# Kernel optimization log

Measured on AMD Instinct MI355X. Metric: run time of the kernel, lower is better.

Reference implementation:

```python
import jax, jax.numpy as jnp
import numpy as np

N, E = 20000, 4096
IN_DIM, DET_DIM, HID, OUT = 512, 256, 256, 2
HALF = HID // 2
EPS = 1e-6


def setup_inputs() -> dict:
    key = jax.random.key(0)
    ks = jax.random.split(key, 20)
    g = lambda k, shape, fan_in: jax.random.normal(k, shape, jnp.float32) / np.sqrt(fan_in)
    return {
        "x": jax.random.normal(ks[0], (N, IN_DIM), jnp.float32),
        "z": jax.random.normal(ks[1], (N, DET_DIM), jnp.float32),
        "incidence": jax.random.uniform(ks[2], (N, E), jnp.float32),
        "edge_weights": jax.random.uniform(ks[3], (E,), jnp.float32),
        "psi_w": g(ks[4], (IN_DIM, HALF), IN_DIM), "psi_b": jnp.zeros((HALF,), jnp.float32),
        "phi_w": g(ks[5], (DET_DIM, HALF), DET_DIM), "phi_b": jnp.zeros((HALF,), jnp.float32),
        "g1_w": g(ks[6], (2 * HALF, HID), 2 * HALF), "g1_b": jnp.zeros((HID,), jnp.float32),
        "g2_w": g(ks[7], (HID, HALF), HID), "g2_b": jnp.zeros((HALF,), jnp.float32),
        "th1": g(ks[8], (HALF, HID), HALF), "b1": jnp.zeros((HID,), jnp.float32),
        "th2": g(ks[9], (HID, HID), HID), "b2": jnp.zeros((HID,), jnp.float32),
        "out_w": g(ks[10], (HID, OUT), HID), "out_b": jnp.zeros((OUT,), jnp.float32),
    }


def hconv(X, H, w, theta, bias):
    # HGNN-style message passing: Dv^{-1/2} H W De^{-1} H^T Dv^{-1/2} (X theta) + b
    Xt = X @ theta                              # [N,F]
    De = H.sum(axis=0)                          # [E] edge degree
    Dv = H @ w                                  # [N] weighted node degree
    inv_sqrt_dv = jax.lax.rsqrt(jnp.maximum(Dv, EPS))[:, None]
    He = H.T @ (Xt * inv_sqrt_dv)               # [E,F] gather to hyperedges
    He = He * (w / jnp.maximum(De, EPS))[:, None]
    return (H @ He) * inv_sqrt_dv + bias        # scatter back to nodes


def reference(x, z, incidence, edge_weights,
              psi_w, psi_b, phi_w, phi_b,
              g1_w, g1_b, g2_w, g2_b,
              th1, b1, th2, b2, out_w, out_b):
    proj_x = x @ psi_w + psi_b                  # [N,HALF]
    proj_z = z @ phi_w + phi_b                  # [N,HALF]
    cat = jnp.concatenate([proj_x, proj_z], axis=1)
    gate = jax.nn.sigmoid(jax.nn.relu(cat @ g1_w + g1_b) @ g2_w + g2_b)
    fused = gate * proj_z + (1.0 - gate) * proj_x
    h = jax.nn.relu(hconv(fused, incidence, edge_weights, th1, b1))
    h = jax.nn.relu(hconv(h, incidence, edge_weights, th2, b2))
    logits = h @ out_w + out_b                  # [N,OUT]
    return logits, gate
```

## Files before the change

kernel.cpp:

```cpp
#include <hip/hip_runtime.h>
#include <hip/hip_bf16.h>


typedef __bf16 bf16_t;
typedef __attribute__((ext_vector_type(8))) __bf16 bf16x8;
typedef __attribute__((ext_vector_type(4))) __bf16 bf16x4;
typedef __attribute__((ext_vector_type(4))) float f32x4;

#define NN 20000
#define NE 4096
#define NNP 20480
#define AT_S 16
#define NEB 16
#define NNB 160

__device__ __forceinline__ f32x4 mfma16(bf16x8 a, bf16x8 b, f32x4 c) {
  return __builtin_amdgcn_mfma_f32_16x16x32_bf16(a, b, c, 0, 0, 0);
}

__global__ __launch_bounds__(256) void stats_cvt_kern(const float* __restrict__ H,
                                                      const float* __restrict__ w,
                                                      float* __restrict__ Dvp,
                                                      float* __restrict__ Dep,
                                                      bf16_t* __restrict__ Hbp) {
  __shared__ float dvl2[128][65];
  __shared__ float deP[4][256];
  int t = threadIdx.x, l = t & 63, wv = t >> 6;
  long e0 = (long)blockIdx.x * 256;
  long n0 = (long)blockIdx.y * 128;
  long pbase = ((e0 >> 6) + (l >> 4)) * (long)NNP;
  int inner = (l & 15) * 4;
  f32x4 w4 = *(const f32x4*)(w + e0 + l * 4);
  f32x4 de; de[0] = de[1] = de[2] = de[3] = 0.f;
  #pragma unroll 4
  for (int i = 0; i < 32; ++i) {
    long row = n0 + wv * 32 + i;
    float s;
    if (row < NN) {
      f32x4 u = *(const f32x4*)(H + row * NE + e0 + l * 4);
      bf16x4 pk;
      #pragma unroll
      for (int j = 0; j < 4; ++j) pk[j] = (__bf16)u[j];
      *(bf16x4*)(Hbp + (pbase + row) * 64 + inner) = pk;
      de += u;
      s = u[0] * w4[0] + u[1] * w4[1] + u[2] * w4[2] + u[3] * w4[3];
    } else {
      bf16x4 z;
      #pragma unroll
      for (int j = 0; j < 4; ++j) z[j] = (__bf16)0.f;
      *(bf16x4*)(Hbp + (pbase + row) * 64 + inner) = z;
      s = 0.f;
    }
    dvl2[wv * 32 + i][l] = s;
  }
  *(f32x4*)(&deP[wv][l * 4]) = de;
  __syncthreads();
  {
    int row = t >> 1, hf = t & 1;
    float s = 0.f;
    #pragma unroll
    for (int j = 0; j < 32; ++j) s += dvl2[row][hf * 32 + j];
    s += __shfl_xor(s, 1);
    if (hf == 0) Dvp[(long)blockIdx.x * NNP + n0 + row] = s;
  }
  {
    float s = deP[0][t] + deP[1][t] + deP[2][t] + deP[3][t];
    Dep[(long)blockIdx.y * NE + e0 + t] = s;
  }
}

__global__ __launch_bounds__(256) void finalize_kern(const float* __restrict__ Dvp,
                                                     const float* __restrict__ Dep,
                                                     const float* __restrict__ w,
                                                     float* __restrict__ isd,
                                                     float* __restrict__ es) {
  int t = blockIdx.x * 256 + threadIdx.x;
  if (t < NN) {
    float s = 0.f;
    #pragma unroll 8
    for (int b = 0; b < NEB; ++b) s += Dvp[(long)b * NNP + t];
    isd[t] = rsqrtf(fmaxf(s, 1e-6f));
  }
  if (t < NE) {
    float s = 0.f;
    #pragma unroll 8
    for (int b = 0; b < NNB; ++b) s += Dep[(long)b * NE + t];
    es[t] = w[t] / fmaxf(s, 1e-6f);
  }
}

__global__ void cvtw_kern(const float* __restrict__ psi, const float* __restrict__ phi,
                          const float* __restrict__ g1,  const float* __restrict__ g2,
                          const float* __restrict__ th1, const float* __restrict__ th2,
                          bf16_t* dpsi, bf16_t* dphi, bf16_t* dg1, bf16_t* dg2,
                          bf16_t* dth1, bf16_t* dth2) {
  int t = blockIdx.x * 256 + threadIdx.x;
  if (t < 65536) {
    int nc = t >> 9, k = t & 511; dpsi[t] = (__bf16)psi[k * 128 + nc];
  } else if (t < 98304) {
    int i = t - 65536; int nc = i >> 8, k = i & 255; dphi[i] = (__bf16)phi[k * 128 + nc];
  } else if (t < 163840) {
    int i = t - 98304; int nc = i >> 8, k = i & 255; dg1[i] = (__bf16)g1[k * 256 + nc];
  } else if (t < 196608) {
    int i = t - 163840; int nc = i >> 8, k = i & 255; dg2[i] = (__bf16)g2[k * 128 + nc];
  } else if (t < 229376) {
    int i = t - 196608; int nc = i >> 7, k = i & 127; dth1[i] = (__bf16)th1[k * 256 + nc];
  } else if (t < 294912) {
    int i = t - 229376; int nc = i >> 8, k = i & 255; dth2[i] = (__bf16)th2[k * 256 + nc];
  }
}

enum { EPI_CAT = 0, EPI_RELU = 1 };

template<bool AF32, int EPI>
__global__ __launch_bounds__(256) void gemm_node_kern(
    const void* __restrict__ Av, int lda, const bf16_t* __restrict__ Bt, int K,
    const float* __restrict__ bias, bf16_t* __restrict__ dst, int ldc) {
  int tid = threadIdx.x, l = tid & 63, wv = tid >> 6;
  int lr = l & 15, lq = l >> 4;
  int hm = wv >> 1;
  int mo = blockIdx.x * 32 + hm * 16;
  int no = blockIdx.y * 128 + (wv & 1) * 64;
  f32x4 acc[4] = {};
  for (int k0 = 0; k0 < K; k0 += 32) {
    int row = mo + lr;
    bf16x8 a;
    if (row < NN) {
      if constexpr (AF32) {
        const float* ap = (const float*)Av + (long)row * lda + k0 + lq * 8;
        f32x4 u0 = *(const f32x4*)ap, u1 = *(const f32x4*)(ap + 4);
        #pragma unroll
        for (int j = 0; j < 4; ++j) { a[j] = (__bf16)u0[j]; a[j + 4] = (__bf16)u1[j]; }
      } else {
        a = *(const bf16x8*)((const bf16_t*)Av + (long)row * lda + k0 + lq * 8);
      }
    } else {
      #pragma unroll
      for (int j = 0; j < 8; ++j) a[j] = (__bf16)0.f;
    }
    #pragma unroll
    for (int ni = 0; ni < 4; ++ni) {
      bf16x8 b = *(const bf16x8*)(Bt + (long)(no + ni * 16 + lr) * K + k0 + lq * 8);
      acc[ni] = mfma16(a, b, acc[ni]);
    }
  }
  #pragma unroll
  for (int ni = 0; ni < 4; ++ni) {
    int colf = no + ni * 16 + lr;
    int rb = mo + lq * 4;
    f32x4 v = acc[ni];
    float bs = bias[colf];
    for (int r = 0; r < 4; ++r) {
      int n = rb + r;
      if (n < NN) {
        float xx = v[r] + bs;
        if constexpr (EPI == EPI_RELU) xx = xx > 0.f ? xx : 0.f;
        dst[(long)n * ldc + colf] = (__bf16)xx;
      }
    }
  }
}

__global__ __launch_bounds__(256) void gate_y_kern(
    const bf16_t* __restrict__ hid1, const bf16_t* __restrict__ g2w,
    const float* __restrict__ g2b, const bf16_t* __restrict__ cat,
    const bf16_t* __restrict__ th1w, const float* __restrict__ isd,
    float* __restrict__ gate_out, bf16_t* __restrict__ Yf) {
  __shared__ bf16_t fl[32 * 132];
  int t = threadIdx.x, l = t & 63, wv = t >> 6;
  int lr = l & 15, lq = l >> 4;
  if (blockIdx.x >= 625) {
    bf16x8 z;
    #pragma unroll
    for (int j = 0; j < 8; ++j) z[j] = (__bf16)0.f;
    #pragma unroll
    for (int i = 0; i < 4; ++i)
      *(bf16x8*)(Yf + (((long)(wv + i * 4) * 640 + blockIdx.x) * 64 + l) * 8) = z;
    return;
  }
  long n0 = (long)blockIdx.x * 32;
  int hm = wv >> 1, nq = wv & 1;
  int mo = hm * 16, no = nq * 64;
  f32x4 acc[4] = {};
  for (int k0 = 0; k0 < 256; k0 += 32) {
    bf16x8 a = *(const bf16x8*)(hid1 + (n0 + mo + lr) * 256 + k0 + lq * 8);
    #pragma unroll
    for (int ni = 0; ni < 4; ++ni) {
      bf16x8 b = *(const bf16x8*)(g2w + (long)(no + ni * 16 + lr) * 256 + k0 + lq * 8);
      acc[ni] = mfma16(a, b, acc[ni]);
    }
  }
  #pragma unroll
  for (int ni = 0; ni < 4; ++ni) {
    int colf = no + ni * 16 + lr;
    float bs = g2b[colf];
    #pragma unroll
    for (int r = 0; r < 4; ++r) {
      long n = n0 + mo + lq * 4 + r;
      float g = 1.f / (1.f + __expf(-(acc[ni][r] + bs)));
      gate_out[n * 128 + colf] = g;
      float px = (float)cat[n * 256 + colf];
      float pz = (float)cat[n * 256 + 128 + colf];
      fl[(mo + lq * 4 + r) * 132 + colf] = (__bf16)(g * pz + (1.f - g) * px);
    }
  }
  __syncthreads();
  int hm2 = wv >> 1, f128 = (wv & 1) * 128;
  f32x4 acc2[8] = {};
  for (int k0 = 0; k0 < 128; k0 += 32) {
    bf16x8 a = *(const bf16x8*)(fl + (hm2 * 16 + lr) * 132 + k0 + lq * 8);
    #pragma unroll
    for (int ni = 0; ni < 8; ++ni) {
      bf16x8 b = *(const bf16x8*)(th1w + (long)(f128 + ni * 16 + lr) * 128 + k0 + lq * 8);
      acc2[ni] = mfma16(a, b, acc2[ni]);
    }
  }
  int lanep = (hm2 * 2 + (lq >> 1)) * 16 + lr;
  #pragma unroll
  for (int ni = 0; ni < 8; ++ni) {
    int fblk = (f128 >> 4) + ni;
    bf16x4 pk;
    #pragma unroll
    for (int r = 0; r < 4; ++r) {
      long n = n0 + hm2 * 16 + lq * 4 + r;
      pk[r] = (__bf16)(acc2[ni][r] * isd[n]);
    }
    *(bf16x4*)(Yf + (((long)fblk * 640 + blockIdx.x) * 64 + lanep) * 8 + (lq & 1) * 4) = pk;
  }
}

__global__ __launch_bounds__(512) void at_gemm_kern(const bf16_t* __restrict__ Hbp,
                                                    const bf16_t* __restrict__ Yf,
                                                    bf16_t* __restrict__ part) {
  __shared__ bf16_t T[128 * 72];
  int t = threadIdx.x, l = t & 63, wv = t >> 6;
  int lr = l & 15, lq = l >> 4;
  int eh = wv >> 2, fq = wv & 3;
  int e0 = blockIdx.x * 128;
  int s0 = blockIdx.y * 20, s1 = s0 + 20;
  int rp = t >> 4;
  int ck = t & 15;
  f32x4 acc[4][4] = {};
  const bf16_t* src = Hbp + (((long)(e0 >> 6) + (ck >> 3)) * NNP + (long)s0 * 64 + 2 * rp) * 64
                          + (ck & 7) * 8;
  bf16x8 ra = *(const bf16x8*)src;
  bf16x8 rb = *(const bf16x8*)(src + 64);
  for (int s = s0; s < s1; ++s) {
    __syncthreads();
    #pragma unroll
    for (int j = 0; j < 8; ++j) {
      int jj = (j + ck) & 7;
      int el = ck * 8 + jj;
      unsigned lo = (unsigned)__builtin_bit_cast(unsigned short, (__bf16)ra[jj]);
      unsigned hi = (unsigned)__builtin_bit_cast(unsigned short, (__bf16)rb[jj]);
      *(unsigned*)(T + el * 72 + rp * 2) = lo | (hi << 16);
    }
    __syncthreads();
    if (s + 1 < s1) {
      src += 64 * 64;
      ra = *(const bf16x8*)src;
      rb = *(const bf16x8*)(src + 64);
    }
    #pragma unroll
    for (int k32 = 0; k32 < 2; ++k32) {
      bf16x8 a[4], b[4];
      #pragma unroll
      for (int ni = 0; ni < 4; ++ni)
        a[ni] = *(const bf16x8*)(T + (eh * 64 + ni * 16 + lr) * 72 + k32 * 32 + lq * 8);
      const bf16_t* bp = Yf + ((long)(s * 2 + k32) * 64 + l) * 8;
      #pragma unroll
      for (int ni = 0; ni < 4; ++ni)
        b[ni] = *(const bf16x8*)(bp + (long)(fq * 4 + ni) * 640 * 512);
      #pragma unroll
      for (int ae = 0; ae < 4; ++ae)
        #pragma unroll
        for (int bf = 0; bf < 4; ++bf)
          acc[ae][bf] = mfma16(a[ae], b[bf], acc[ae][bf]);
    }
  }
  bf16_t* pp = part + (long)blockIdx.y * (256 * 4096);
  #pragma unroll
  for (int ae = 0; ae < 4; ++ae) {
    int eblk16 = (e0 >> 4) + eh * 4 + ae;
    #pragma unroll
    for (int bf = 0; bf < 4; ++bf) {
      int fblk = fq * 4 + bf;
      f32x4 v = acc[ae][bf];
      bf16x4 pk;
      for (int r = 0; r < 4; ++r) pk[r] = (__bf16)v[r];
      *(bf16x4*)(pp + (((long)eblk16 * 16 + fblk) * 64 + l) * 4) = pk;
    }
  }
}

__global__ __launch_bounds__(256) void reduce_he(const bf16_t* __restrict__ part,
                                                 const float* __restrict__ es,
                                                 bf16_t* __restrict__ Hef) {
  int u = blockIdx.x * 256 + threadIdx.x;
  int lane = u & 63, tile = u >> 6;
  int fblk = tile & 15, eblk16 = tile >> 4;
  int lr = lane & 15, lq = lane >> 4;
  int e_base = eblk16 * 16 + lq * 4;
  float a0 = 0.f, a1 = 0.f, a2 = 0.f, a3 = 0.f;
  #pragma unroll
  for (int s = 0; s < AT_S; ++s) {
    bf16x4 v = *(const bf16x4*)(part + (long)s * (256 * 4096) + (long)u * 4);
    a0 += (float)v[0]; a1 += (float)v[1]; a2 += (float)v[2]; a3 += (float)v[3];
  }
  f32x4 e4 = *(const f32x4*)(es + e_base);
  bf16x4 pk;
  pk[0] = (__bf16)(a0 * e4[0]); pk[1] = (__bf16)(a1 * e4[1]);
  pk[2] = (__bf16)(a2 * e4[2]); pk[3] = (__bf16)(a3 * e4[3]);
  int eblk32 = eblk16 >> 1;
  int lanep = ((eblk16 & 1) * 2 + (lq >> 1)) * 16 + lr;
  long slot = (((long)fblk * 128 + eblk32) * 64 + lanep) * 8 + (lq & 1) * 4;
  *(bf16x4*)(Hef + slot) = pk;
}

template<int CONV>
__global__ __launch_bounds__(512) void out_gemm_kern(const bf16_t* __restrict__ Hef,
                                                     const bf16_t* __restrict__ Hbp,
                                                     const float* __restrict__ isd,
                                                     const float* __restrict__ bias,
                                                     const bf16_t* __restrict__ th2w,
                                                     bf16_t* __restrict__ Yf,
                                                     const float* __restrict__ ow,
                                                     const float* __restrict__ ob,
                                                     float* __restrict__ out) {
  __shared__ bf16_t lbuf[2][4096];
  __shared__ float lgp[8][64][2];
  __shared__ bf16_t hl[64 * 260];
  int t = threadIdx.x, l = t & 63, wv = t >> 6;
  int lr = l & 15, lq = l >> 4;
  long r0 = (long)blockIdx.x * 64;
  f32x4 acc[4][2] = {};
  const bf16_t* asrc = Hbp + (r0 + (wv >> 1) * 16 + lr) * 64 + (wv & 1) * 32 + lq * 8;
  const bf16_t* bbase = Hef + (long)l * 8;
  bf16x8 rg = *(const bf16x8*)asrc;
  int c = 0;
  for (int s = 0; s < 64; ++s) {
    *(bf16x8*)(&lbuf[c][wv * 512 + l * 8]) = rg;
    __syncthreads();
    if (s + 1 < 64) rg = *(const bf16x8*)(asrc + (long)(s + 1) * NNP * 64);
    #pragma unroll
    for (int k32 = 0; k32 < 2; ++k32) {
      bf16x8 a[4], b[2];
      #pragma unroll
      for (int mi = 0; mi < 4; ++mi)
        a[mi] = *(const bf16x8*)(&lbuf[c][(mi * 2 + k32) * 512 + l * 8]);
      int eblk = s * 2 + k32;
      #pragma unroll
      for (int ni = 0; ni < 2; ++ni)
        b[ni] = *(const bf16x8*)(bbase + ((long)(wv * 2 + ni) * 128 + eblk) * 512);
      #pragma unroll
      for (int mi = 0; mi < 4; ++mi) {
        acc[mi][0] = mfma16(a[mi], b[0], acc[mi][0]);
        acc[mi][1] = mfma16(a[mi], b[1], acc[mi][1]);
      }
    }
    c ^= 1;
  }
  #pragma unroll
  for (int mi = 0; mi < 4; ++mi) {
    long nb = r0 + mi * 16 + lq * 4;
    #pragma unroll
    for (int r = 0; r < 4; ++r) {
      long n = nb + r;
      float sd = (n < NN) ? isd[n] : 0.f;
      float a0 = 0.f, a1 = 0.f;
      #pragma unroll
      for (int ni = 0; ni < 2; ++ni) {
        int f = wv * 32 + ni * 16 + lr;
        float vv = acc[mi][ni][r] * sd + bias[f];
        vv = vv > 0.f ? vv : 0.f;
        if constexpr (CONV == 1) {
          hl[(mi * 16 + lq * 4 + r) * 260 + f] = (__bf16)vv;
        } else {
          a0 += vv * ow[f * 2];
          a1 += vv * ow[f * 2 + 1];
        }
      }
      if constexpr (CONV == 2) {
        #pragma unroll
        for (int m = 1; m < 16; m <<= 1) { a0 += __shfl_xor(a0, m); a1 += __shfl_xor(a1, m); }
        if (lr == 0) {
          int rowl = mi * 16 + lq * 4 + r;
          lgp[wv][rowl][0] = a0;
          lgp[wv][rowl][1] = a1;
        }
      }
    }
  }
  if constexpr (CONV == 1) {
    __syncthreads();
    int nh = wv >> 2, fq = wv & 3;
    f32x4 acc2[2][4] = {};
    for (int k0 = 0; k0 < 256; k0 += 32) {
      bf16x8 a0v = *(const bf16x8*)(hl + (nh * 32 + lr) * 260 + k0 + lq * 8);
      bf16x8 a1v = *(const bf16x8*)(hl + (nh * 32 + 16 + lr) * 260 + k0 + lq * 8);
      #pragma unroll
      for (int ni = 0; ni < 4; ++ni) {
        bf16x8 b = *(const bf16x8*)(th2w + (long)(fq * 64 + ni * 16 + lr) * 256 + k0 + lq * 8);
        acc2[0][ni] = mfma16(a0v, b, acc2[0][ni]);
        acc2[1][ni] = mfma16(a1v, b, acc2[1][ni]);
      }
    }
    long nblk = blockIdx.x * 2 + nh;
    #pragma unroll
    for (int mi = 0; mi < 2; ++mi) {
      int lanep = (mi * 2 + (lq >> 1)) * 16 + lr;
      #pragma unroll
      for (int ni = 0; ni < 4; ++ni) {
        int fblk = fq * 4 + ni;
        bf16x4 pk;
        #pragma unroll
        for (int r = 0; r < 4; ++r) {
          long n = r0 + nh * 32 + mi * 16 + lq * 4 + r;
          float sc = (n < NN) ? isd[n] : 0.f;
          pk[r] = (__bf16)(acc2[mi][ni][r] * sc);
        }
        *(bf16x4*)(Yf + (((long)fblk * 640 + nblk) * 64 + lanep) * 8 + (lq & 1) * 4) = pk;
      }
    }
  } else {
    __syncthreads();
    if (t < 64) {
      float s0 = 0.f, s1 = 0.f;
      #pragma unroll
      for (int wvi = 0; wvi < 8; ++wvi) { s0 += lgp[wvi][t][0]; s1 += lgp[wvi][t][1]; }
      long n = r0 + t;
      if (n < NN) {
        out[n * 2]     = s0 + ob[0];
        out[n * 2 + 1] = s1 + ob[1];
      }
    }
  }
}

extern "C" void kernel_launch(void* const* d_in, const int* in_sizes, int n_in,
                              void* d_out, int out_size, void* d_ws, size_t ws_size,
                              hipStream_t stream) {
  const float* x    = (const float*)d_in[0];
  const float* z    = (const float*)d_in[1];
  const float* H    = (const float*)d_in[2];
  const float* w    = (const float*)d_in[3];
  const float* psi_w = (const float*)d_in[4];
  const float* psi_b = (const float*)d_in[5];
  const float* phi_w = (const float*)d_in[6];
  const float* phi_b = (const float*)d_in[7];
  const float* g1_w  = (const float*)d_in[8];
  const float* g1_b  = (const float*)d_in[9];
  const float* g2_w  = (const float*)d_in[10];
  const float* g2_b  = (const float*)d_in[11];
  const float* th1   = (const float*)d_in[12];
  const float* b1    = (const float*)d_in[13];
  const float* th2   = (const float*)d_in[14];
  const float* b2    = (const float*)d_in[15];
  const float* out_w = (const float*)d_in[16];
  const float* out_b = (const float*)d_in[17];

  float* logits_out = (float*)d_out;
  float* gate_out   = logits_out + (size_t)NN * 2;

  char* p = (char*)d_ws;
  auto alloc = [&](size_t bytes) { char* r = p; p += (bytes + 255) & ~(size_t)255; return r; };
  float* Dvp  = (float*)alloc((size_t)NEB * NNP * 4);
  float* Dep  = (float*)alloc((size_t)NNB * NE * 4);
  float* isd  = (float*)alloc((size_t)NN * 4);
  float* es   = (float*)alloc((size_t)NE * 4);
  bf16_t* cat   = (bf16_t*)alloc((size_t)NN * 256 * 2);
  bf16_t* hid1  = (bf16_t*)alloc((size_t)NN * 256 * 2);
  bf16_t* Yf    = (bf16_t*)alloc((size_t)16 * 640 * 512 * 2);
  bf16_t* Hef   = (bf16_t*)alloc((size_t)16 * 128 * 512 * 2);
  bf16_t* pbuf  = (bf16_t*)alloc((size_t)AT_S * 256 * 4096 * 2);
  bf16_t* Hbp   = (bf16_t*)alloc((size_t)NNP * NE * 2);
  bf16_t* psi_wt = (bf16_t*)alloc(65536 * 2);
  bf16_t* phi_wt = (bf16_t*)alloc(32768 * 2);
  bf16_t* g1_wt  = (bf16_t*)alloc(65536 * 2);
  bf16_t* g2_wt  = (bf16_t*)alloc(32768 * 2);
  bf16_t* th1_wt = (bf16_t*)alloc(32768 * 2);
  bf16_t* th2_wt = (bf16_t*)alloc(65536 * 2);

  cvtw_kern<<<1152, 256, 0, stream>>>(psi_w, phi_w, g1_w, g2_w, th1, th2,
                                      psi_wt, phi_wt, g1_wt, g2_wt, th1_wt, th2_wt);
  stats_cvt_kern<<<dim3(NEB, NNB), 256, 0, stream>>>(H, w, Dvp, Dep, Hbp);
  finalize_kern<<<79, 256, 0, stream>>>(Dvp, Dep, w, isd, es);

  gemm_node_kern<true,  EPI_CAT ><<<dim3(625, 1), 256, 0, stream>>>(x, 512, psi_wt, 512, psi_b, cat,       256);
  gemm_node_kern<true,  EPI_CAT ><<<dim3(625, 1), 256, 0, stream>>>(z, 256, phi_wt, 256, phi_b, cat + 128, 256);
  gemm_node_kern<false, EPI_RELU><<<dim3(625, 2), 256, 0, stream>>>(cat, 256, g1_wt, 256, g1_b, hid1, 256);
  gate_y_kern<<<640, 256, 0, stream>>>(hid1, g2_wt, g2_b, cat, th1_wt, isd, gate_out, Yf);

  at_gemm_kern<<<dim3(32, AT_S), 512, 0, stream>>>(Hbp, Yf, pbuf);
  reduce_he<<<1024, 256, 0, stream>>>(pbuf, es, Hef);
  out_gemm_kern<1><<<320, 512, 0, stream>>>(Hef, Hbp, isd, b1, th2_wt, Yf,
                                            nullptr, nullptr, nullptr);

  at_gemm_kern<<<dim3(32, AT_S), 512, 0, stream>>>(Hbp, Yf, pbuf);
  reduce_he<<<1024, 256, 0, stream>>>(pbuf, es, Hef);
  out_gemm_kern<2><<<320, 512, 0, stream>>>(Hef, Hbp, isd, b2, nullptr, nullptr,
                                            out_w, out_b, logits_out);

  (void)in_sizes; (void)n_in; (void)out_size; (void)ws_size;
}
```

Before: 580.3 us.

## Enlarge stats tile to 512 edges and out-GEMM row tile to 80 nodes

The stats/convert kernel now covers 512 edges per block, halving the number of Dv partials, and reduces Dv within quads by shuffle before the shared-memory sum. The output GEMM processes 80 rows per block instead of 64, so 256 blocks match the CU count and each Hef B-fragment load is reused across five M tiles. The fused th2 GEMM is remapped so each wave handles all 80 rows and 32 output features. The cost is more registers and LDS per block, plus uneven A-tile loading across waves.

```diff
diff --git a/kernel.cpp b/kernel.cpp
--- a/kernel.cpp
+++ b/kernel.cpp
@@ -11,7 +11,7 @@
 #define NE 4096
 #define NNP 20480
 #define AT_S 16
-#define NEB 16
+#define NEB 8
 #define NNB 160
 
 __device__ __forceinline__ f32x4 mfma16(bf16x8 a, bf16x8 b, f32x4 c) {
@@ -23,49 +23,59 @@
                                                       float* __restrict__ Dvp,
                                                       float* __restrict__ Dep,
                                                       bf16_t* __restrict__ Hbp) {
-  __shared__ float dvl2[128][65];
-  __shared__ float deP[4][256];
+  __shared__ float dvl[128][17];
+  __shared__ float deP[4][512];
   int t = threadIdx.x, l = t & 63, wv = t >> 6;
-  long e0 = (long)blockIdx.x * 256;
+  long e0 = (long)blockIdx.x * 512;
   long n0 = (long)blockIdx.y * 128;
-  long pbase = ((e0 >> 6) + (l >> 4)) * (long)NNP;
+  long pA = ((e0 >> 6) + (l >> 4)) * (long)NNP;
+  long pB = pA + 4 * (long)NNP;
   int inner = (l & 15) * 4;
-  f32x4 w4 = *(const f32x4*)(w + e0 + l * 4);
-  f32x4 de; de[0] = de[1] = de[2] = de[3] = 0.f;
+  f32x4 wa = *(const f32x4*)(w + e0 + l * 4);
+  f32x4 wb = *(const f32x4*)(w + e0 + 256 + l * 4);
+  f32x4 dea; dea[0] = dea[1] = dea[2] = dea[3] = 0.f;
+  f32x4 deb; deb[0] = deb[1] = deb[2] = deb[3] = 0.f;
   #pragma unroll 4
   for (int i = 0; i < 32; ++i) {
     long row = n0 + wv * 32 + i;
     float s;
     if (row < NN) {
-      f32x4 u = *(const f32x4*)(H + row * NE + e0 + l * 4);
-      bf16x4 pk;
-      #pragma unroll
-      for (int j = 0; j < 4; ++j) pk[j] = (__bf16)u[j];
-      *(bf16x4*)(Hbp + (pbase + row) * 64 + inner) = pk;
-      de += u;
-      s = u[0] * w4[0] + u[1] * w4[1] + u[2] * w4[2] + u[3] * w4[3];
+      f32x4 ua = *(const f32x4*)(H + row * NE + e0 + l * 4);
+      f32x4 ub = *(const f32x4*)(H + row * NE + e0 + 256 + l * 4);
+      bf16x4 pa, pb;
+      #pragma unroll
+      for (int j = 0; j < 4; ++j) { pa[j] = (__bf16)ua[j]; pb[j] = (__bf16)ub[j]; }
+      *(bf16x4*)(Hbp + (pA + row) * 64 + inner) = pa;
+      *(bf16x4*)(Hbp + (pB + row) * 64 + inner) = pb;
+      dea += ua; deb += ub;
+      s = ua[0]*wa[0] + ua[1]*wa[1] + ua[2]*wa[2] + ua[3]*wa[3]
+        + ub[0]*wb[0] + ub[1]*wb[1] + ub[2]*wb[2] + ub[3]*wb[3];
     } else {
       bf16x4 z;
       #pragma unroll
       for (int j = 0; j < 4; ++j) z[j] = (__bf16)0.f;
-      *(bf16x4*)(Hbp + (pbase + row) * 64 + inner) = z;
+      *(bf16x4*)(Hbp + (pA + row) * 64 + inner) = z;
+      *(bf16x4*)(Hbp + (pB + row) * 64 + inner) = z;
       s = 0.f;
     }
-    dvl2[wv * 32 + i][l] = s;
-  }
-  *(f32x4*)(&deP[wv][l * 4]) = de;
+    s += __shfl_xor(s, 1);
+    s += __shfl_xor(s, 2);
+    if ((l & 3) == 0) dvl[wv * 32 + i][l >> 2] = s;
+  }
+  *(f32x4*)(&deP[wv][l * 4]) = dea;
+  *(f32x4*)(&deP[wv][256 + l * 4]) = deb;
   __syncthreads();
+  if (t < 128) {
+    float s = 0.f;
+    #pragma unroll
+    for (int j = 0; j < 16; ++j) s += dvl[t][j];
+    Dvp[(long)blockIdx.x * NNP + n0 + t] = s;
+  }
   {
-    int row = t >> 1, hf = t & 1;
-    float s = 0.f;
-    #pragma unroll
-    for (int j = 0; j < 32; ++j) s += dvl2[row][hf * 32 + j];
-    s += __shfl_xor(s, 1);
-    if (hf == 0) Dvp[(long)blockIdx.x * NNP + n0 + row] = s;
-  }
-  {
-    float s = deP[0][t] + deP[1][t] + deP[2][t] + deP[3][t];
-    Dep[(long)blockIdx.y * NE + e0 + t] = s;
+    float s0 = deP[0][t] + deP[1][t] + deP[2][t] + deP[3][t];
+    float s1 = deP[0][256 + t] + deP[1][256 + t] + deP[2][256 + t] + deP[3][256 + t];
+    Dep[(long)blockIdx.y * NE + e0 + t] = s0;
+    Dep[(long)blockIdx.y * NE + e0 + 256 + t] = s1;
   }
 }
 
@@ -77,7 +87,7 @@
   int t = blockIdx.x * 256 + threadIdx.x;
   if (t < NN) {
     float s = 0.f;
-    #pragma unroll 8
+    #pragma unroll
     for (int b = 0; b < NEB; ++b) s += Dvp[(long)b * NNP + t];
     isd[t] = rsqrtf(fmaxf(s, 1e-6f));
   }
@@ -327,33 +337,42 @@
                                                      const float* __restrict__ ow,
                                                      const float* __restrict__ ob,
                                                      float* __restrict__ out) {
-  __shared__ bf16_t lbuf[2][4096];
-  __shared__ float lgp[8][64][2];
-  __shared__ bf16_t hl[64 * 260];
+  __shared__ bf16_t lbuf[2][5120];
+  __shared__ float lgp[8][80][2];
+  __shared__ bf16_t hl[80 * 260];
   int t = threadIdx.x, l = t & 63, wv = t >> 6;
   int lr = l & 15, lq = l >> 4;
-  long r0 = (long)blockIdx.x * 64;
-  f32x4 acc[4][2] = {};
-  const bf16_t* asrc = Hbp + (r0 + (wv >> 1) * 16 + lr) * 64 + (wv & 1) * 32 + lq * 8;
+  long r0 = (long)blockIdx.x * 80;
+  f32x4 acc[5][2] = {};
+  int f1 = wv, f2 = 8 + wv;
+  bool has2 = wv < 2;
+  const bf16_t* asrc1 = Hbp + (r0 + (f1 >> 1) * 16 + lr) * 64 + (f1 & 1) * 32 + lq * 8;
+  const bf16_t* asrc2 = Hbp + (r0 + (f2 >> 1) * 16 + lr) * 64 + (f2 & 1) * 32 + lq * 8;
   const bf16_t* bbase = Hef + (long)l * 8;
-  bf16x8 rg = *(const bf16x8*)asrc;
+  bf16x8 rg1 = *(const bf16x8*)asrc1;
+  bf16x8 rg2;
+  if (has2) rg2 = *(const bf16x8*)asrc2;
   int c = 0;
   for (int s = 0; s < 64; ++s) {
-    *(bf16x8*)(&lbuf[c][wv * 512 + l * 8]) = rg;
+    *(bf16x8*)(&lbuf[c][f1 * 512 + l * 8]) = rg1;
+    if (has2) *(bf16x8*)(&lbuf[c][f2 * 512 + l * 8]) = rg2;
     __syncthreads();
-    if (s + 1 < 64) rg = *(const bf16x8*)(asrc + (long)(s + 1) * NNP * 64);
+    if (s + 1 < 64) {
+      rg1 = *(const bf16x8*)(asrc1 + (long)(s + 1) * NNP * 64);
+      if (has2) rg2 = *(const bf16x8*)(asrc2 + (long)(s + 1) * NNP * 64);
+    }
     #pragma unroll
     for (int k32 = 0; k32 < 2; ++k32) {
-      bf16x8 a[4], b[2];
-      #pragma unroll
-      for (int mi = 0; mi < 4; ++mi)
+      bf16x8 a[5], b[2];
+      #pragma unroll
+      for (int mi = 0; mi < 5; ++mi)
         a[mi] = *(const bf16x8*)(&lbuf[c][(mi * 2 + k32) * 512 + l * 8]);
       int eblk = s * 2 + k32;
       #pragma unroll
       for (int ni = 0; ni < 2; ++ni)
         b[ni] = *(const bf16x8*)(bbase + ((long)(wv * 2 + ni) * 128 + eblk) * 512);
       #pragma unroll
-      for (int mi = 0; mi < 4; ++mi) {
+      for (int mi = 0; mi < 5; ++mi) {
         acc[mi][0] = mfma16(a[mi], b[0], acc[mi][0]);
         acc[mi][1] = mfma16(a[mi], b[1], acc[mi][1]);
       }
@@ -361,7 +380,7 @@
     c ^= 1;
   }
   #pragma unroll
-  for (int mi = 0; mi < 4; ++mi) {
+  for (int mi = 0; mi < 5; ++mi) {
     long nb = r0 + mi * 16 + lq * 4;
     #pragma unroll
     for (int r = 0; r < 4; ++r) {
@@ -393,29 +412,34 @@
   }
   if constexpr (CONV == 1) {
     __syncthreads();
-    int nh = wv >> 2, fq = wv & 3;
-    f32x4 acc2[2][4] = {};
+    f32x4 acc2[5][2] = {};
     for (int k0 = 0; k0 < 256; k0 += 32) {
-      bf16x8 a0v = *(const bf16x8*)(hl + (nh * 32 + lr) * 260 + k0 + lq * 8);
-      bf16x8 a1v = *(const bf16x8*)(hl + (nh * 32 + 16 + lr) * 260 + k0 + lq * 8);
-      #pragma unroll
-      for (int ni = 0; ni < 4; ++ni) {
-        bf16x8 b = *(const bf16x8*)(th2w + (long)(fq * 64 + ni * 16 + lr) * 256 + k0 + lq * 8);
-        acc2[0][ni] = mfma16(a0v, b, acc2[0][ni]);
-        acc2[1][ni] = mfma16(a1v, b, acc2[1][ni]);
-      }
-    }
-    long nblk = blockIdx.x * 2 + nh;
-    #pragma unroll
-    for (int mi = 0; mi < 2; ++mi) {
-      int lanep = (mi * 2 + (lq >> 1)) * 16 + lr;
-      #pragma unroll
-      for (int ni = 0; ni < 4; ++ni) {
-        int fblk = fq * 4 + ni;
+      bf16x8 a_[5], b2[2];
+      #pragma unroll
+      for (int mi = 0; mi < 5; ++mi)
+        a_[mi] = *(const bf16x8*)(hl + (mi * 16 + lr) * 260 + k0 + lq * 8);
+      #pragma unroll
+      for (int ni = 0; ni < 2; ++ni)
+        b2[ni] = *(const bf16x8*)(th2w + (long)(wv * 32 + ni * 16 + lr) * 256 + k0 + lq * 8);
+      #pragma unroll
+      for (int mi = 0; mi < 5; ++mi) {
+        acc2[mi][0] = mfma16(a_[mi], b2[0], acc2[mi][0]);
+        acc2[mi][1] = mfma16(a_[mi], b2[1], acc2[mi][1]);
+      }
+    }
+    #pragma unroll
+    for (int mi = 0; mi < 5; ++mi) {
+      long nbase = r0 + mi * 16;
+      long nblk = nbase >> 5;
+      int hm16 = (int)((nbase >> 4) & 1);
+      int lanep = (hm16 * 2 + (lq >> 1)) * 16 + lr;
+      #pragma unroll
+      for (int ni = 0; ni < 2; ++ni) {
+        int fblk = wv * 2 + ni;
         bf16x4 pk;
         #pragma unroll
         for (int r = 0; r < 4; ++r) {
-          long n = r0 + nh * 32 + mi * 16 + lq * 4 + r;
+          long n = nbase + lq * 4 + r;
           float sc = (n < NN) ? isd[n] : 0.f;
           pk[r] = (__bf16)(acc2[mi][ni][r] * sc);
         }
@@ -424,7 +448,7 @@
     }
   } else {
     __syncthreads();
-    if (t < 64) {
+    if (t < 80) {
       float s0 = 0.f, s1 = 0.f;
       #pragma unroll
       for (int wvi = 0; wvi < 8; ++wvi) { s0 += lgp[wvi][t][0]; s1 += lgp[wvi][t][1]; }
@@ -493,12 +517,12 @@
 
   at_gemm_kern<<<dim3(32, AT_S), 512, 0, stream>>>(Hbp, Yf, pbuf);
   reduce_he<<<1024, 256, 0, stream>>>(pbuf, es, Hef);
-  out_gemm_kern<1><<<320, 512, 0, stream>>>(Hef, Hbp, isd, b1, th2_wt, Yf,
+  out_gemm_kern<1><<<256, 512, 0, stream>>>(Hef, Hbp, isd, b1, th2_wt, Yf,
                                             nullptr, nullptr, nullptr);
 
   at_gemm_kern<<<dim3(32, AT_S), 512, 0, stream>>>(Hbp, Yf, pbuf);
   reduce_he<<<1024, 256, 0, stream>>>(pbuf, es, Hef);
-  out_gemm_kern<2><<<320, 512, 0, stream>>>(Hef, Hbp, isd, b2, nullptr, nullptr,
+  out_gemm_kern<2><<<256, 512, 0, stream>>>(Hef, Hbp, isd, b2, nullptr, nullptr,
                                             out_w, out_b, logits_out);
 
   (void)in_sizes; (void)n_in; (void)out_size; (void)ws_size;
```

Result: faster. 537.1 us (-7.4%).
